# Performance work log

Measured on AMD Instinct MI355X. Metric: run time of the kernel, lower is better.

The kernel has to match this reference:

```python
import jax, jax.numpy as jnp
import numpy as np

H_FULL, W_FULL = 256, 704
IMG_H, IMG_W = 16, 44  # height//16, width//16
D_BINS, D_STR, D_END = 50, 1.0, 45.0
N_CAMS = 6
BEV_C = 192
VOX_STR = np.array([-40.0, -40.0, -1.0], np.float32)
VOX_END = np.array([40.0, 40.0, 5.4], np.float32)


def _frustum():
    # Faithful to create_pixel_grid: x/y built width-major, flattened, then flat-reshaped
    # to (img_h, img_w) in forward (this scrambling is intentional / matches torch .reshape).
    x = jnp.broadcast_to(jnp.linspace(0.0, W_FULL - 1.0, IMG_W)[:, None], (IMG_W, IMG_H))
    y = jnp.broadcast_to(jnp.linspace(0.0, H_FULL - 1.0, IMG_H)[None, :], (IMG_W, IMG_H))
    pix = jnp.stack([x, y], 0).reshape(2, IMG_H, IMG_W)
    pix = jnp.broadcast_to(pix[:, None], (2, D_BINS, IMG_H, IMG_W))
    d = jnp.broadcast_to(jnp.linspace(D_STR, D_END, D_BINS)[None, :, None, None], (1, D_BINS, IMG_H, IMG_W))
    return jnp.transpose(jnp.concatenate([pix, d], 0), (1, 2, 3, 0))  # [D, h, w, 3]


def trilinear_sample(vol, grid):
    # vol [B,C,D,H,W]; grid [B,Do,Ho,Wo,3] normalized (x,y,z); align_corners=True, zeros padding
    B, C, D, H, W = vol.shape
    Do, Ho, Wo = grid.shape[1:4]
    g = grid.reshape(B, -1, 3)
    P = g.shape[1]
    x = (g[..., 0] + 1.0) * 0.5 * (W - 1)
    y = (g[..., 1] + 1.0) * 0.5 * (H - 1)
    z = (g[..., 2] + 1.0) * 0.5 * (D - 1)
    x0f, y0f, z0f = jnp.floor(x), jnp.floor(y), jnp.floor(z)
    fx, fy, fz = x - x0f, y - y0f, z - z0f
    x0, y0, z0 = x0f.astype(jnp.int32), y0f.astype(jnp.int32), z0f.astype(jnp.int32)
    vol_flat = vol.reshape(B, C, D * H * W)
    gather = jax.vmap(lambda vf, i: jnp.take(vf, i, axis=1))
    out = jnp.zeros((B, C, P), vol.dtype)
    for dz in (0, 1):
        wz = fz if dz else 1.0 - fz
        iz = z0 + dz
        for dy in (0, 1):
            wy = fy if dy else 1.0 - fy
            iy = y0 + dy
            for dx in (0, 1):
                wx = fx if dx else 1.0 - fx
                ix = x0 + dx
                valid = (ix >= 0) & (ix < W) & (iy >= 0) & (iy < H) & (iz >= 0) & (iz < D)
                idx = (jnp.clip(iz, 0, D - 1) * H + jnp.clip(iy, 0, H - 1)) * W + jnp.clip(ix, 0, W - 1)
                v = gather(vol_flat, idx)  # [B,C,P]
                out = out + v * (wx * wy * wz * valid)[:, None, :]
    return out.reshape(B, C, Do, Ho, Wo)


def conv3x3(x, w, b):
    y = jax.lax.conv_general_dilated(x, w, window_strides=(1, 1), padding='SAME',
                                     dimension_numbers=('NCHW', 'OIHW', 'NCHW'))
    return y + b[None, :, None, None]


def setup_inputs() -> dict:
    key = jax.random.key(0)
    ks = jax.random.split(key, 10)
    B = 2
    eye3 = jnp.eye(3, dtype=jnp.float32)
    eye4 = jnp.eye(4, dtype=jnp.float32)
    bev_feat = jax.random.normal(ks[0], (B, BEV_C, 100, 100, 8), jnp.float32)
    imgs = jax.random.normal(ks[1], (B, N_CAMS, 3, H_FULL, W_FULL), jnp.float32)
    sensor2egos = eye4 + 0.1 * jax.random.normal(ks[2], (B, N_CAMS, 4, 4), jnp.float32)
    ego2globals = eye4 + 0.1 * jax.random.normal(ks[3], (B, N_CAMS, 4, 4), jnp.float32)
    K = jnp.array([[700.0, 0.0, 352.0], [0.0, 700.0, 128.0], [0.0, 0.0, 1.0]], jnp.float32)
    intrins = K + 1.0 * jax.random.normal(ks[4], (B, N_CAMS, 3, 3), jnp.float32)
    post_rots = eye3 + 0.01 * jax.random.normal(ks[5], (B, N_CAMS, 3, 3), jnp.float32)
    post_trans = 0.1 * jax.random.normal(ks[6], (B, N_CAMS, 3), jnp.float32)
    bda = eye3 + 0.01 * jax.random.normal(ks[7], (B, 3, 3), jnp.float32)
    enc = BEV_C * D_BINS  # 9600
    conv1_w = 0.003 * jax.random.normal(ks[8], (256, enc, 3, 3), jnp.float32)
    conv1_b = jnp.zeros((256,), jnp.float32)
    conv2_w = 0.02 * jax.random.normal(ks[9], (88, 256, 3, 3), jnp.float32)
    conv2_b = jnp.zeros((88,), jnp.float32)
    return dict(bev_feat=bev_feat, imgs=imgs, sensor2egos=sensor2egos, ego2globals=ego2globals,
                intrins=intrins, post_rots=post_rots, post_trans=post_trans, bda=bda,
                conv1_w=conv1_w, conv1_b=conv1_b, conv2_w=conv2_w, conv2_b=conv2_b)


def reference(bev_feat, imgs, sensor2egos, ego2globals, intrins, post_rots, post_trans, bda,
              conv1_w, conv1_b, conv2_w, conv2_b):
    B = imgs.shape[0]
    vol = jnp.transpose(bev_feat, (0, 1, 4, 3, 2))  # [B,C,Z,Y,X] -> grid_sample (x=W, y=H, z=D)
    fr = _frustum()[None, None]  # [1,1,D,h,w,3]
    pts = fr - post_trans[:, :, None, None, None, :]  # [B,6,D,h,w,3]
    pts = jnp.einsum('bnij,bndhwj->bndhwi', jnp.linalg.inv(post_rots), pts)
    pts = jnp.concatenate([pts[..., :2] * pts[..., 2:3], pts[..., 2:3]], -1)
    pts = jnp.einsum('bnij,bndhwj->bndhwi', jnp.linalg.inv(intrins[:, :N_CAMS]), pts)
    N = D_BINS * IMG_H * IMG_W
    cam = pts.reshape(B, N_CAMS, 3, N)  # faithful flat reshape (same semantics as torch .reshape)
    cam = jnp.concatenate([cam, jnp.ones((B, N_CAMS, 1, N), cam.dtype)], 2)
    ego = jnp.einsum('bnij,bnjp->bnip', sensor2egos[:, :N_CAMS, :3, :], cam)
    ego = jnp.einsum('bij,bnjp->bnip', bda, ego)
    g = jnp.transpose(ego, (0, 1, 3, 2))  # [B,6,N,3]
    vs = jnp.asarray(VOX_STR)
    vl = jnp.asarray(VOX_END - VOX_STR)
    g = (g - vs) / vl * 2.0 - 1.0
    g = g.reshape(B, N_CAMS * D_BINS, IMG_H, IMG_W, 3)  # batch all cams into the depth axis
    s = trilinear_sample(vol, g)  # [B,C,6*D,h,w]
    s = s.reshape(B, BEV_C, N_CAMS, D_BINS, IMG_H, IMG_W)
    s = jnp.transpose(s, (0, 2, 1, 3, 4, 5)).reshape(B * N_CAMS, BEV_C * D_BINS, IMG_H, IMG_W)
    x = jax.nn.relu(conv3x3(s, conv1_w, conv1_b))
    x = jax.nn.relu(conv3x3(x, conv2_w, conv2_b))
    return x  # [B*6, 88, 16, 44] == stack(dim=1).flatten(0,1)
```

## Files before the change

kernel.cpp:

```cpp
#include <hip/hip_runtime.h>
#include <hip/hip_bf16.h>
#include <stdint.h>

typedef __attribute__((ext_vector_type(8))) short s16x8;
typedef __attribute__((ext_vector_type(4))) float f32x4;
#define BF16 __hip_bfloat16

__device__ __forceinline__ void gload16(void* lds, const void* g) {
  __builtin_amdgcn_global_load_lds((const __attribute__((address_space(1))) void*)g,
                                   (__attribute__((address_space(3))) void*)lds, 16, 0, 0);
}

__device__ __forceinline__ void inv3(const float* m, float* o) {
  float a00=m[0],a01=m[1],a02=m[2],a10=m[3],a11=m[4],a12=m[5],a20=m[6],a21=m[7],a22=m[8];
  float c00 = a11*a22 - a12*a21;
  float c01 = a12*a20 - a10*a22;
  float c02 = a10*a21 - a11*a20;
  float det = a00*c00 + a01*c01 + a02*c02;
  float id = 1.0f/det;
  o[0]=c00*id; o[1]=(a02*a21-a01*a22)*id; o[2]=(a01*a12-a02*a11)*id;
  o[3]=c01*id; o[4]=(a00*a22-a02*a20)*id; o[5]=(a02*a10-a00*a12)*id;
  o[6]=c02*id; o[7]=(a01*a20-a00*a21)*id; o[8]=(a00*a11-a01*a10)*id;
}

__global__ __launch_bounds__(192) void k_prep_vol(const float* __restrict__ bev, BF16* __restrict__ volT) {
  int blk = blockIdx.x;
  int b = blk / 10000, xy = blk % 10000;
  int t = threadIdx.x;
  __shared__ alignas(16) BF16 sm[1536];
  const float* src = bev + (((size_t)b*192 + t)*10000 + xy)*8;
#pragma unroll
  for (int z = 0; z < 8; ++z) sm[z*192 + t] = __float2bfloat16(src[z]);
  __syncthreads();
  BF16* dst = volT + (size_t)blk*1536;
  *reinterpret_cast<s16x8*>(&dst[t*8]) = *reinterpret_cast<const s16x8*>(&sm[t*8]);
}

__global__ __launch_bounds__(256) void k_prep_w1(const float* __restrict__ w1, BF16* __restrict__ A1) {
  unsigned o = blockIdx.x*256u + threadIdx.x;
  unsigned oc = o / 86400u; unsigned r = o % 86400u;
  unsigned seg = r / 9600u; unsigned r2 = r % 9600u;
  unsigned dd = r2 / 192u;  unsigned c  = r2 % 192u;
  unsigned in = (oc*9600u + c*50u + dd)*9u + seg;
  A1[o] = __float2bfloat16(w1[in]);
}

__global__ __launch_bounds__(256) void k_prep_w2(const float* __restrict__ w2, BF16* __restrict__ w2T) {
  unsigned o = blockIdx.x*256u + threadIdx.x;
  unsigned oc = o / 2304u; unsigned r = o % 2304u;
  unsigned seg = r / 256u; unsigned c = r % 256u;
  float v = (oc < 88u) ? w2[(oc*256u + c)*9u + seg] : 0.0f;
  w2T[o] = __float2bfloat16(v);
}

__global__ __launch_bounds__(256) void k_geom(const float* __restrict__ s2e, const float* __restrict__ intr,
                       const float* __restrict__ prots, const float* __restrict__ ptrans,
                       const float* __restrict__ bda, float* __restrict__ geom) {
  int tid = blockIdx.x*256 + threadIdx.x;
  int p = tid % 35200; int bn = tid / 35200;
  int b = bn / 6;
  float PR[9], IN[9], iPR[9], iIN[9], BD[9], SE[12], PT[3];
#pragma unroll
  for (int i = 0; i < 9; ++i) { PR[i] = prots[bn*9+i]; IN[i] = intr[bn*9+i]; BD[i] = bda[b*9+i]; }
#pragma unroll
  for (int i = 0; i < 12; ++i) SE[i] = s2e[bn*16+i];
#pragma unroll
  for (int i = 0; i < 3; ++i) PT[i] = ptrans[bn*3+i];
  inv3(PR, iPR); inv3(IN, iIN);
  float cam[3];
#pragma unroll
  for (int c3 = 0; c3 < 3; ++c3) {
    int f = c3*35200 + p;
    int comp = f % 3; int t1 = f / 3;
    int w = t1 % 44;  int t2 = t1 / 44;
    int h = t2 % 16;  int dd = t2 / 16;
    int hw = h*44 + w;
    float px = 703.0f*(float)(hw >> 4)*(1.0f/43.0f);
    float py = 17.0f*(float)(hw & 15);
    float dv = 1.0f + 44.0f*(float)dd*(1.0f/49.0f);
    float t0 = px - PT[0], t1f = py - PT[1], t2f = dv - PT[2];
    float ux = iPR[0]*t0 + iPR[1]*t1f + iPR[2]*t2f;
    float uy = iPR[3]*t0 + iPR[4]*t1f + iPR[5]*t2f;
    float uz = iPR[6]*t0 + iPR[7]*t1f + iPR[8]*t2f;
    float m0 = ux*uz, m1 = uy*uz, m2 = uz;
    cam[c3] = iIN[comp*3+0]*m0 + iIN[comp*3+1]*m1 + iIN[comp*3+2]*m2;
  }
  float e0 = SE[0]*cam[0] + SE[1]*cam[1] + SE[2]*cam[2] + SE[3];
  float e1 = SE[4]*cam[0] + SE[5]*cam[1] + SE[6]*cam[2] + SE[7];
  float e2 = SE[8]*cam[0] + SE[9]*cam[1] + SE[10]*cam[2] + SE[11];
  float q0 = BD[0]*e0 + BD[1]*e1 + BD[2]*e2;
  float q1 = BD[3]*e0 + BD[4]*e1 + BD[5]*e2;
  float q2 = BD[6]*e0 + BD[7]*e1 + BD[8]*e2;
  float gx = (q0 + 40.0f)*(1.0f/80.0f)*2.0f - 1.0f;
  float gy = (q1 + 40.0f)*(1.0f/80.0f)*2.0f - 1.0f;
  float gz = (q2 + 1.0f)*(1.0f/6.4f)*2.0f - 1.0f;
  float* o = geom + (size_t)tid*3;
  o[0] = (gx + 1.0f)*0.5f*99.0f;
  o[1] = (gy + 1.0f)*0.5f*99.0f;
  o[2] = (gz + 1.0f)*0.5f*7.0f;
}

__global__ __launch_bounds__(256) void k_sample(const BF16* __restrict__ volT, const float* __restrict__ geom,
                         BF16* __restrict__ s_p) {
  unsigned tid = blockIdx.x*256u + threadIdx.x;
  unsigned c = tid % 192u; unsigned q = tid / 192u;
  unsigned pix = q % 704u; unsigned q2 = q / 704u;
  unsigned dd = q2 % 50u;  unsigned bn = q2 / 50u;
  unsigned b = bn / 6u;
  const float* g = geom + ((size_t)bn*35200 + dd*704 + pix)*3;
  float X = g[0], Y = g[1], Z = g[2];
  float xf = floorf(X), yf = floorf(Y), zf = floorf(Z);
  int x0 = (int)xf, y0 = (int)yf, z0 = (int)zf;
  float fx = X - xf, fy = Y - yf, fz = Z - zf;
  float acc = 0.0f;
#pragma unroll
  for (int dz = 0; dz < 2; ++dz) {
    int iz = z0 + dz; float wz = dz ? fz : 1.0f - fz;
    bool vz = (iz >= 0) && (iz < 8);
    int cz = min(max(iz, 0), 7);
#pragma unroll
    for (int dy = 0; dy < 2; ++dy) {
      int iy = y0 + dy; float wy = dy ? fy : 1.0f - fy;
      bool vy = vz && (iy >= 0) && (iy < 100);
      int cy = min(max(iy, 0), 99);
#pragma unroll
      for (int dx = 0; dx < 2; ++dx) {
        int ix = x0 + dx; float wx = dx ? fx : 1.0f - fx;
        bool vv = vy && (ix >= 0) && (ix < 100);
        int cx = min(max(ix, 0), 99);
        float wgt = wx*wy*wz;
        if (vv && wgt != 0.0f) {
          size_t a = ((((size_t)b*100 + cx)*100 + cy)*8 + cz)*192 + c;
          acc += wgt * __bfloat162float(volT[a]);
        }
      }
    }
  }
  s_p[((size_t)bn*704 + pix)*9600 + dd*192 + c] = __float2bfloat16(acc);
}

__global__ __launch_bounds__(256) void k_gemm1(const BF16* __restrict__ A1, const BF16* __restrict__ s_p,
                        const BF16* __restrict__ zpage, float* __restrict__ part) {
  int gid = blockIdx.x;
  int ks = gid % 12; int t0 = gid / 12;
  int nt = t0 % 6;   t0 /= 6;
  int mt = t0 & 1;   int bn = t0 >> 1;
  int oc0 = mt*128, pix0 = nt*128;
  int tid = threadIdx.x, wv = tid >> 6, lane = tid & 63;
  int wr = wv >> 1, wc = wv & 1;
  __shared__ alignas(16) short lA[4096];
  __shared__ alignas(16) short lB[4096];
  int rsub = lane >> 2, kcol = (lane & 3)*8;
  int lr = lane & 15, kh8 = (lane >> 4)*8;
  int k = ks*7200, kend = k + 7200;
  int arow0 = (wv*2+0)*16 + rsub;
  int arow1 = (wv*2+1)*16 + rsub;
  const BF16* gA0 = A1 + (size_t)(oc0 + arow0)*86400 + k + kcol;
  const BF16* gA1 = A1 + (size_t)(oc0 + arow1)*86400 + k + kcol;
  short* ldsA0 = &lA[(wv*2+0)*512];
  short* ldsA1 = &lA[(wv*2+1)*512];
  short* ldsB0 = &lB[(wv*2+0)*512];
  short* ldsB1 = &lB[(wv*2+1)*512];
  int prow0 = pix0 + (wv*2+0)*16 + rsub;
  int prow1 = pix0 + (wv*2+1)*16 + rsub;
  int ph00 = prow0/44, pw00 = prow0%44;
  int ph10 = prow1/44, pw10 = prow1%44;
  f32x4 acc[4][4] = {};
  while (k < kend) {
    int seg = k / 9600;
    int kloc = k - seg*9600;
    int rem0 = 9600 - kloc, rem1 = kend - k;
    int nsteps = ((rem0 < rem1) ? rem0 : rem1) >> 5;
    int dh = seg/3 - 1, dw = seg%3 - 1;
    const BF16 *gB0, *gB1; int inc0, inc1;
    {
      int ph = ph00 + dh, pw = pw00 + dw;
      bool v = (prow0 < 704) && (ph >= 0) && (ph < 16) && (pw >= 0) && (pw < 44);
      gB0 = v ? s_p + ((size_t)bn*704 + ph*44 + pw)*9600 + kloc + kcol : zpage + kcol;
      inc0 = v ? 32 : 0;
    }
    {
      int ph = ph10 + dh, pw = pw10 + dw;
      bool v = (prow1 < 704) && (ph >= 0) && (ph < 16) && (pw >= 0) && (pw < 44);
      gB1 = v ? s_p + ((size_t)bn*704 + ph*44 + pw)*9600 + kloc + kcol : zpage + kcol;
      inc1 = v ? 32 : 0;
    }
    for (int s = 0; s < nsteps; ++s) {
      __syncthreads();
      gload16(ldsA0, gA0); gload16(ldsA1, gA1);
      gload16(ldsB0, gB0); gload16(ldsB1, gB1);
      __syncthreads();
      s16x8 af[4], bfr[4];
#pragma unroll
      for (int m = 0; m < 4; ++m)
        af[m] = *reinterpret_cast<const s16x8*>(&lA[(wr*64 + m*16 + lr)*32 + kh8]);
#pragma unroll
      for (int n = 0; n < 4; ++n)
        bfr[n] = *reinterpret_cast<const s16x8*>(&lB[(wc*64 + n*16 + lr)*32 + kh8]);
#pragma unroll
      for (int m = 0; m < 4; ++m)
#pragma unroll
        for (int n = 0; n < 4; ++n)
          acc[m][n] = __builtin_amdgcn_mfma_f32_16x16x32_bf16(af[m], bfr[n], acc[m][n], 0, 0, 0);
      gA0 += 32; gA1 += 32; gB0 += inc0; gB1 += inc1;
    }
    k += nsteps*32;
  }
#pragma unroll
  for (int m = 0; m < 4; ++m) {
    int ocb = oc0 + wr*64 + m*16 + ((lane >> 4) << 2);
#pragma unroll
    for (int n = 0; n < 4; ++n) {
      int px = pix0 + wc*64 + n*16 + lr;
      if (px < 704) {
        float* dst = part + (((size_t)ks*12 + bn)*256 + ocb)*704 + px;
#pragma unroll
        for (int r = 0; r < 4; ++r) dst[(size_t)r*704] = acc[m][n][r];
      }
    }
  }
}

__global__ __launch_bounds__(256) void k_reduce1(const float* __restrict__ part, const float* __restrict__ b1,
                          BF16* __restrict__ out1p) {
  int bn = blockIdx.x / 44; int pg = blockIdx.x % 44; int pix0 = pg*16;
  int t = threadIdx.x;
  __shared__ float sm[4096];
  for (int f = t; f < 4096; f += 256) {
    int oc = f >> 4, pl = f & 15;
    float s = 0.0f;
#pragma unroll
    for (int ks = 0; ks < 12; ++ks)
      s += part[(((size_t)ks*12 + bn)*256 + oc)*704 + pix0 + pl];
    s += b1[oc];
    sm[f] = fmaxf(s, 0.0f);
  }
  __syncthreads();
  for (int f = t; f < 4096; f += 256) {
    int pl = f >> 8;
    int oc = f & 255;
    out1p[((size_t)bn*704 + pix0 + pl)*256 + oc] = __float2bfloat16(sm[oc*16 + pl]);
  }
}

__global__ __launch_bounds__(256) void k_gemm2(const BF16* __restrict__ w2T, const BF16* __restrict__ x1,
                        const BF16* __restrict__ zpage, const float* __restrict__ b2,
                        float* __restrict__ out) {
  int gid = blockIdx.x;
  int nt = gid % 11, bn = gid / 11;
  int pix0 = nt*64;
  int tid = threadIdx.x, wv = tid >> 6, lane = tid & 63;
  int wr = wv >> 1, wc = wv & 1;
  __shared__ alignas(16) short lA[3072];
  __shared__ alignas(16) short lB[2048];
  int rsub = lane >> 2, kcol = (lane & 3)*8;
  int lr = lane & 15, kh8 = (lane >> 4)*8;
  int ar0 = wv*16 + rsub;
  int ar1 = (wv+4)*16 + rsub;
  const BF16* gA0 = w2T + (size_t)ar0*2304 + kcol;
  const BF16* gA1 = w2T + (size_t)ar1*2304 + kcol;
  short* lA0 = &lA[wv*512];
  short* lA1 = &lA[(wv+4)*512];
  short* lB0 = &lB[wv*512];
  int prow = pix0 + wv*16 + rsub;
  int ph0 = prow/44, pw0 = prow%44;
  f32x4 acc[3][2] = {};
  for (int seg = 0; seg < 9; ++seg) {
    int dh = seg/3 - 1, dw = seg%3 - 1;
    int ph = ph0 + dh, pw = pw0 + dw;
    bool v = (ph >= 0) && (ph < 16) && (pw >= 0) && (pw < 44);
    const BF16* gB = v ? x1 + ((size_t)bn*704 + ph*44 + pw)*256 + kcol : zpage + kcol;
    int incB = v ? 32 : 0;
#pragma unroll
    for (int s = 0; s < 8; ++s) {
      __syncthreads();
      gload16(lA0, gA0);
      if (wv < 2) gload16(lA1, gA1);
      gload16(lB0, gB);
      __syncthreads();
      s16x8 af[3], bfr[2];
#pragma unroll
      for (int m = 0; m < 3; ++m)
        af[m] = *reinterpret_cast<const s16x8*>(&lA[(wr*48 + m*16 + lr)*32 + kh8]);
#pragma unroll
      for (int n = 0; n < 2; ++n)
        bfr[n] = *reinterpret_cast<const s16x8*>(&lB[(wc*32 + n*16 + lr)*32 + kh8]);
#pragma unroll
      for (int m = 0; m < 3; ++m)
#pragma unroll
        for (int n = 0; n < 2; ++n)
          acc[m][n] = __builtin_amdgcn_mfma_f32_16x16x32_bf16(af[m], bfr[n], acc[m][n], 0, 0, 0);
      gA0 += 32; gA1 += 32; gB += incB;
    }
  }
#pragma unroll
  for (int m = 0; m < 3; ++m) {
    int ocb = wr*48 + m*16 + ((lane >> 4) << 2);
#pragma unroll
    for (int n = 0; n < 2; ++n) {
      int px = pix0 + wc*32 + n*16 + lr;
#pragma unroll
      for (int r = 0; r < 4; ++r) {
        int oc = ocb + r;
        if (oc < 88)
          out[((size_t)bn*88 + oc)*704 + px] = fmaxf(acc[m][n][r] + b2[oc], 0.0f);
      }
    }
  }
}

extern "C" void kernel_launch(void* const* d_in, const int* in_sizes, int n_in,
                              void* d_out, int out_size, void* d_ws, size_t ws_size,
                              hipStream_t stream) {
  (void)in_sizes; (void)n_in; (void)out_size;
  const float* bev   = (const float*)d_in[0];
  const float* s2e   = (const float*)d_in[2];
  const float* intr  = (const float*)d_in[4];
  const float* prots = (const float*)d_in[5];
  const float* ptrns = (const float*)d_in[6];
  const float* bda   = (const float*)d_in[7];
  const float* w1    = (const float*)d_in[8];
  const float* b1    = (const float*)d_in[9];
  const float* w2    = (const float*)d_in[10];
  const float* b2    = (const float*)d_in[11];
  float* out = (float*)d_out;

  char* ws = (char*)d_ws;
  size_t off = 0;
  BF16*  volT  = (BF16*)(ws + off);  off += 61440000;
  BF16*  A1    = (BF16*)(ws + off);  off += 44236800;
  BF16*  w2T   = (BF16*)(ws + off);  off += 442368;
  float* geom  = (float*)(ws + off); off += 5068800;
  BF16*  s_p   = (BF16*)(ws + off);  off += 162201600;
  float* part  = (float*)(ws + off); off += 103809024;
  BF16*  out1p = (BF16*)(ws + off);  off += 4325376;
  BF16*  zpage = (BF16*)(ws + off);  off += 4096;
  if (off > ws_size) return;

  hipMemsetAsync(zpage, 0, 4096, stream);

  k_prep_vol<<<20000, 192, 0, stream>>>(bev, volT);
  k_prep_w1 <<<86400, 256, 0, stream>>>(w1, A1);
  k_prep_w2 <<<864,   256, 0, stream>>>(w2, w2T);
  k_geom    <<<1650,  256, 0, stream>>>(s2e, intr, prots, ptrns, bda, geom);
  k_sample  <<<316800,256, 0, stream>>>(volT, geom, s_p);
  k_gemm1   <<<1728,  256, 0, stream>>>(A1, s_p, zpage, part);
  k_reduce1 <<<528,   256, 0, stream>>>(part, b1, out1p);
  k_gemm2   <<<132,   256, 0, stream>>>(w2T, out1p, zpage, b2, out);
}
```

Measured before the change: 1.206 ms.

## Double-buffer gemm1, vectorize sampling and weight prep, store fp16 partials

```diff
diff --git a/kernel.cpp b/kernel.cpp
--- a/kernel.cpp
+++ b/kernel.cpp
@@ -1,14 +1,21 @@
 #include <hip/hip_runtime.h>
 #include <hip/hip_bf16.h>
+#include <hip/hip_fp16.h>
 #include <stdint.h>
 
 typedef __attribute__((ext_vector_type(8))) short s16x8;
 typedef __attribute__((ext_vector_type(4))) float f32x4;
 #define BF16 __hip_bfloat16
 
+#define VM0 asm volatile("s_waitcnt vmcnt(0)" ::: "memory")
+
 __device__ __forceinline__ void gload16(void* lds, const void* g) {
   __builtin_amdgcn_global_load_lds((const __attribute__((address_space(1))) void*)g,
                                    (__attribute__((address_space(3))) void*)lds, 16, 0, 0);
+}
+
+__device__ __forceinline__ short f2bf(float f) {
+  union { __hip_bfloat16 h; short s; } u; u.h = __float2bfloat16(f); return u.s;
 }
 
 __device__ __forceinline__ void inv3(const float* m, float* o) {
@@ -37,12 +44,36 @@
 }
 
 __global__ __launch_bounds__(256) void k_prep_w1(const float* __restrict__ w1, BF16* __restrict__ A1) {
-  unsigned o = blockIdx.x*256u + threadIdx.x;
-  unsigned oc = o / 86400u; unsigned r = o % 86400u;
-  unsigned seg = r / 9600u; unsigned r2 = r % 9600u;
-  unsigned dd = r2 / 192u;  unsigned c  = r2 % 192u;
-  unsigned in = (oc*9600u + c*50u + dd)*9u + seg;
-  A1[o] = __float2bfloat16(w1[in]);
+  int blk = blockIdx.x;
+  int oc = blk / 6, c0 = (blk % 6) * 32;
+  __shared__ short sm[18000];
+  int t = threadIdx.x;
+  const float* src = w1 + (size_t)oc*86400 + (size_t)c0*450;
+  for (int i = 0; i < 15; ++i) {
+    int f4 = i*256 + t;
+    if (f4 < 3600) {
+      float4 v = *((const float4*)src + f4);
+      int flat = f4*4;
+#pragma unroll
+      for (int q = 0; q < 4; ++q) {
+        int fl = flat + q;
+        int c = fl / 450, r = fl % 450, dd = r / 9, sg = r % 9;
+        float vq = (q==0)?v.x:(q==1)?v.y:(q==2)?v.z:v.w;
+        sm[(sg*50 + dd)*40 + c] = f2bf(vq);
+      }
+    }
+  }
+  __syncthreads();
+  BF16* dstbase = A1 + (size_t)oc*86400 + c0;
+  for (int i = 0; i < 8; ++i) {
+    int fw = i*256 + t;
+    if (fw < 1800) {
+      int sdd = fw >> 2, q4 = fw & 3;
+      int sg = sdd / 50, dd = sdd % 50;
+      s16x8 v = *(const s16x8*)&sm[sdd*40 + q4*8];
+      *(s16x8*)&dstbase[(size_t)sg*9600 + dd*192 + q4*8] = v;
+    }
+  }
 }
 
 __global__ __launch_bounds__(256) void k_prep_w2(const float* __restrict__ w2, BF16* __restrict__ w2T) {
@@ -103,16 +134,17 @@
 __global__ __launch_bounds__(256) void k_sample(const BF16* __restrict__ volT, const float* __restrict__ geom,
                          BF16* __restrict__ s_p) {
   unsigned tid = blockIdx.x*256u + threadIdx.x;
-  unsigned c = tid % 192u; unsigned q = tid / 192u;
-  unsigned pix = q % 704u; unsigned q2 = q / 704u;
-  unsigned dd = q2 % 50u;  unsigned bn = q2 / 50u;
+  unsigned cg8 = (tid % 24u) * 8u;
+  unsigned q   = tid / 24u;
+  unsigned dd  = q % 50u;  unsigned q2 = q / 50u;
+  unsigned pix = q2 % 704u; unsigned bn = q2 / 704u;
   unsigned b = bn / 6u;
   const float* g = geom + ((size_t)bn*35200 + dd*704 + pix)*3;
   float X = g[0], Y = g[1], Z = g[2];
   float xf = floorf(X), yf = floorf(Y), zf = floorf(Z);
   int x0 = (int)xf, y0 = (int)yf, z0 = (int)zf;
   float fx = X - xf, fy = Y - yf, fz = Z - zf;
-  float acc = 0.0f;
+  float acc[8] = {0,0,0,0,0,0,0,0};
 #pragma unroll
   for (int dz = 0; dz < 2; ++dz) {
     int iz = z0 + dz; float wz = dz ? fz : 1.0f - fz;
@@ -130,98 +162,101 @@
         int cx = min(max(ix, 0), 99);
         float wgt = wx*wy*wz;
         if (vv && wgt != 0.0f) {
-          size_t a = ((((size_t)b*100 + cx)*100 + cy)*8 + cz)*192 + c;
-          acc += wgt * __bfloat162float(volT[a]);
+          s16x8 v = *(const s16x8*)&volT[((((size_t)b*100 + cx)*100 + cy)*8 + cz)*192 + cg8];
+#pragma unroll
+          for (int j = 0; j < 8; ++j) {
+            unsigned u = (unsigned)(unsigned short)v[j];
+            acc[j] += wgt * __uint_as_float(u << 16);
+          }
         }
       }
     }
   }
-  s_p[((size_t)bn*704 + pix)*9600 + dd*192 + c] = __float2bfloat16(acc);
-}
-
+  s16x8 o;
+#pragma unroll
+  for (int j = 0; j < 8; ++j) o[j] = f2bf(acc[j]);
+  *(s16x8*)&s_p[((size_t)bn*704 + pix)*9600 + dd*192 + cg8] = o;
+}
+
+#define G1_NS 180
 __global__ __launch_bounds__(256) void k_gemm1(const BF16* __restrict__ A1, const BF16* __restrict__ s_p,
-                        const BF16* __restrict__ zpage, float* __restrict__ part) {
+                        const BF16* __restrict__ zpage, __half* __restrict__ part) {
   int gid = blockIdx.x;
-  int ks = gid % 12; int t0 = gid / 12;
+  int ks = gid % 15; int t0 = gid / 15;
   int nt = t0 % 6;   t0 /= 6;
   int mt = t0 & 1;   int bn = t0 >> 1;
   int oc0 = mt*128, pix0 = nt*128;
   int tid = threadIdx.x, wv = tid >> 6, lane = tid & 63;
   int wr = wv >> 1, wc = wv & 1;
-  __shared__ alignas(16) short lA[4096];
-  __shared__ alignas(16) short lB[4096];
-  int rsub = lane >> 2, kcol = (lane & 3)*8;
-  int lr = lane & 15, kh8 = (lane >> 4)*8;
-  int k = ks*7200, kend = k + 7200;
-  int arow0 = (wv*2+0)*16 + rsub;
-  int arow1 = (wv*2+1)*16 + rsub;
-  const BF16* gA0 = A1 + (size_t)(oc0 + arow0)*86400 + k + kcol;
-  const BF16* gA1 = A1 + (size_t)(oc0 + arow1)*86400 + k + kcol;
-  short* ldsA0 = &lA[(wv*2+0)*512];
-  short* ldsA1 = &lA[(wv*2+1)*512];
-  short* ldsB0 = &lB[(wv*2+0)*512];
-  short* ldsB1 = &lB[(wv*2+1)*512];
-  int prow0 = pix0 + (wv*2+0)*16 + rsub;
-  int prow1 = pix0 + (wv*2+1)*16 + rsub;
-  int ph00 = prow0/44, pw00 = prow0%44;
-  int ph10 = prow1/44, pw10 = prow1%44;
+  __shared__ alignas(16) short lA0s[4096], lA1s[4096], lB0s[4096], lB1s[4096];
+  int lr15 = lane & 15, kq8 = (lane >> 4)*8;
+  int k0 = ks*5760;
+  const BF16* gA0 = A1 + (size_t)(oc0 + wv*32 + lr15)*86400 + k0 + kq8;
+  const BF16* gA1 = gA0 + (size_t)16*86400;
+  int prow0 = pix0 + wv*32 + lr15;
+  int prow1 = prow0 + 16;
+  int ph0p = prow0/44, pw0p = prow0%44;
+  int ph1p = prow1/44, pw1p = prow1%44;
+  int seg  = k0 / 9600;
+  int kloc = k0 - seg*9600;
+  const BF16 *gB0, *gB1; int inc0, inc1;
+  {
+    int dh = seg/3 - 1, dw = seg%3 - 1;
+    { int qh = ph0p+dh, qw = pw0p+dw;
+      bool v = (prow0<704)&&(qh>=0)&&(qh<16)&&(qw>=0)&&(qw<44);
+      gB0 = v ? s_p + ((size_t)bn*704 + qh*44+qw)*9600 + kloc + kq8 : zpage + kq8; inc0 = v?32:0; }
+    { int qh = ph1p+dh, qw = pw1p+dw;
+      bool v = (prow1<704)&&(qh>=0)&&(qh<16)&&(qw>=0)&&(qw<44);
+      gB1 = v ? s_p + ((size_t)bn*704 + qh*44+qw)*9600 + kloc + kq8 : zpage + kq8; inc1 = v?32:0; }
+  }
+#define G1_STAGE(LA, LB) { gload16(&LA[wv*1024], gA0); gload16(&LA[wv*1024+512], gA1); \
+                           gload16(&LB[wv*1024], gB0); gload16(&LB[wv*1024+512], gB1); }
+#define G1_BUMP() { gA0 += 32; gA1 += 32; gB0 += inc0; gB1 += inc1; kloc += 32; \
+    if (kloc == 9600) { kloc = 0; seg++; int sg = seg < 9 ? seg : 8; \
+      int dh = sg/3 - 1, dw = sg%3 - 1; \
+      { int qh = ph0p+dh, qw = pw0p+dw; bool v = (prow0<704)&&(qh>=0)&&(qh<16)&&(qw>=0)&&(qw<44); \
+        gB0 = v ? s_p + ((size_t)bn*704 + qh*44+qw)*9600 + kq8 : zpage + kq8; inc0 = v?32:0; } \
+      { int qh = ph1p+dh, qw = pw1p+dw; bool v = (prow1<704)&&(qh>=0)&&(qh<16)&&(qw>=0)&&(qw<44); \
+        gB1 = v ? s_p + ((size_t)bn*704 + qh*44+qw)*9600 + kq8 : zpage + kq8; inc1 = v?32:0; } } }
   f32x4 acc[4][4] = {};
-  while (k < kend) {
-    int seg = k / 9600;
-    int kloc = k - seg*9600;
-    int rem0 = 9600 - kloc, rem1 = kend - k;
-    int nsteps = ((rem0 < rem1) ? rem0 : rem1) >> 5;
-    int dh = seg/3 - 1, dw = seg%3 - 1;
-    const BF16 *gB0, *gB1; int inc0, inc1;
-    {
-      int ph = ph00 + dh, pw = pw00 + dw;
-      bool v = (prow0 < 704) && (ph >= 0) && (ph < 16) && (pw >= 0) && (pw < 44);
-      gB0 = v ? s_p + ((size_t)bn*704 + ph*44 + pw)*9600 + kloc + kcol : zpage + kcol;
-      inc0 = v ? 32 : 0;
-    }
-    {
-      int ph = ph10 + dh, pw = pw10 + dw;
-      bool v = (prow1 < 704) && (ph >= 0) && (ph < 16) && (pw >= 0) && (pw < 44);
-      gB1 = v ? s_p + ((size_t)bn*704 + ph*44 + pw)*9600 + kloc + kcol : zpage + kcol;
-      inc1 = v ? 32 : 0;
-    }
-    for (int s = 0; s < nsteps; ++s) {
-      __syncthreads();
-      gload16(ldsA0, gA0); gload16(ldsA1, gA1);
-      gload16(ldsB0, gB0); gload16(ldsB1, gB1);
-      __syncthreads();
-      s16x8 af[4], bfr[4];
-#pragma unroll
-      for (int m = 0; m < 4; ++m)
-        af[m] = *reinterpret_cast<const s16x8*>(&lA[(wr*64 + m*16 + lr)*32 + kh8]);
-#pragma unroll
-      for (int n = 0; n < 4; ++n)
-        bfr[n] = *reinterpret_cast<const s16x8*>(&lB[(wc*64 + n*16 + lr)*32 + kh8]);
-#pragma unroll
-      for (int m = 0; m < 4; ++m)
-#pragma unroll
-        for (int n = 0; n < 4; ++n)
-          acc[m][n] = __builtin_amdgcn_mfma_f32_16x16x32_bf16(af[m], bfr[n], acc[m][n], 0, 0, 0);
-      gA0 += 32; gA1 += 32; gB0 += inc0; gB1 += inc1;
-    }
-    k += nsteps*32;
+  int ra = wr*2048 + lane*8;
+  int rb = wc*2048 + lane*8;
+#define G1_COMPUTE(LA, LB) { s16x8 af[4], bfv[4]; \
+    _Pragma("unroll") for (int m = 0; m < 4; ++m) af[m]  = *(const s16x8*)&LA[ra + m*512]; \
+    _Pragma("unroll") for (int n = 0; n < 4; ++n) bfv[n] = *(const s16x8*)&LB[rb + n*512]; \
+    _Pragma("unroll") for (int m = 0; m < 4; ++m) \
+    _Pragma("unroll") for (int n = 0; n < 4; ++n) \
+      acc[m][n] = __builtin_amdgcn_mfma_f32_16x16x32_bf16(af[m], bfv[n], acc[m][n], 0, 0, 0); }
+
+  G1_STAGE(lA0s, lB0s); G1_BUMP();
+  VM0;
+  __syncthreads();
+  for (int t = 0; t < G1_NS; t += 2) {
+    G1_STAGE(lA1s, lB1s); G1_BUMP();
+    G1_COMPUTE(lA0s, lB0s);
+    VM0;
+    __syncthreads();
+    if (t + 2 < G1_NS) { G1_STAGE(lA0s, lB0s); G1_BUMP(); }
+    G1_COMPUTE(lA1s, lB1s);
+    VM0;
+    __syncthreads();
   }
 #pragma unroll
   for (int m = 0; m < 4; ++m) {
     int ocb = oc0 + wr*64 + m*16 + ((lane >> 4) << 2);
 #pragma unroll
     for (int n = 0; n < 4; ++n) {
-      int px = pix0 + wc*64 + n*16 + lr;
+      int px = pix0 + wc*64 + n*16 + lr15;
       if (px < 704) {
-        float* dst = part + (((size_t)ks*12 + bn)*256 + ocb)*704 + px;
-#pragma unroll
-        for (int r = 0; r < 4; ++r) dst[(size_t)r*704] = acc[m][n][r];
+        __half* dst = part + (((size_t)ks*12 + bn)*256 + ocb)*704 + px;
+#pragma unroll
+        for (int r = 0; r < 4; ++r) dst[(size_t)r*704] = __float2half(acc[m][n][r]);
       }
     }
   }
 }
 
-__global__ __launch_bounds__(256) void k_reduce1(const float* __restrict__ part, const float* __restrict__ b1,
+__global__ __launch_bounds__(256) void k_reduce1(const __half* __restrict__ part, const float* __restrict__ b1,
                           BF16* __restrict__ out1p) {
   int bn = blockIdx.x / 44; int pg = blockIdx.x % 44; int pix0 = pg*16;
   int t = threadIdx.x;
@@ -230,8 +265,8 @@
     int oc = f >> 4, pl = f & 15;
     float s = 0.0f;
 #pragma unroll
-    for (int ks = 0; ks < 12; ++ks)
-      s += part[(((size_t)ks*12 + bn)*256 + oc)*704 + pix0 + pl];
+    for (int ks = 0; ks < 15; ++ks)
+      s += __half2float(part[(((size_t)ks*12 + bn)*256 + oc)*704 + pix0 + pl]);
     s += b1[oc];
     sm[f] = fmaxf(s, 0.0f);
   }
@@ -253,43 +288,35 @@
   int wr = wv >> 1, wc = wv & 1;
   __shared__ alignas(16) short lA[3072];
   __shared__ alignas(16) short lB[2048];
-  int rsub = lane >> 2, kcol = (lane & 3)*8;
-  int lr = lane & 15, kh8 = (lane >> 4)*8;
-  int ar0 = wv*16 + rsub;
-  int ar1 = (wv+4)*16 + rsub;
-  const BF16* gA0 = w2T + (size_t)ar0*2304 + kcol;
-  const BF16* gA1 = w2T + (size_t)ar1*2304 + kcol;
-  short* lA0 = &lA[wv*512];
-  short* lA1 = &lA[(wv+4)*512];
-  short* lB0 = &lB[wv*512];
-  int prow = pix0 + wv*16 + rsub;
+  int lr15 = lane & 15, kq8 = (lane >> 4)*8;
+  const BF16* gA0 = w2T + (size_t)(wv*16 + lr15)*2304 + kq8;
+  const BF16* gA1 = w2T + (size_t)((4+wv)*16 + lr15)*2304 + kq8;
+  int prow = pix0 + wv*16 + lr15;
   int ph0 = prow/44, pw0 = prow%44;
   f32x4 acc[3][2] = {};
   for (int seg = 0; seg < 9; ++seg) {
     int dh = seg/3 - 1, dw = seg%3 - 1;
-    int ph = ph0 + dh, pw = pw0 + dw;
-    bool v = (ph >= 0) && (ph < 16) && (pw >= 0) && (pw < 44);
-    const BF16* gB = v ? x1 + ((size_t)bn*704 + ph*44 + pw)*256 + kcol : zpage + kcol;
+    int qh = ph0 + dh, qw = pw0 + dw;
+    bool v = (qh >= 0) && (qh < 16) && (qw >= 0) && (qw < 44);
+    const BF16* gB = v ? x1 + ((size_t)bn*704 + qh*44 + qw)*256 + kq8 : zpage + kq8;
     int incB = v ? 32 : 0;
-#pragma unroll
     for (int s = 0; s < 8; ++s) {
       __syncthreads();
-      gload16(lA0, gA0);
-      if (wv < 2) gload16(lA1, gA1);
-      gload16(lB0, gB);
+      gload16(&lA[wv*512], gA0);
+      if (wv < 2) gload16(&lA[(4+wv)*512], gA1);
+      gload16(&lB[wv*512], gB);
+      VM0;
       __syncthreads();
-      s16x8 af[3], bfr[2];
+      s16x8 af[3], bfv[2];
+#pragma unroll
+      for (int m = 0; m < 3; ++m) af[m]  = *(const s16x8*)&lA[(wr*3+m)*512 + lane*8];
+#pragma unroll
+      for (int n = 0; n < 2; ++n) bfv[n] = *(const s16x8*)&lB[(wc*2+n)*512 + lane*8];
 #pragma unroll
       for (int m = 0; m < 3; ++m)
-        af[m] = *reinterpret_cast<const s16x8*>(&lA[(wr*48 + m*16 + lr)*32 + kh8]);
-#pragma unroll
-      for (int n = 0; n < 2; ++n)
-        bfr[n] = *reinterpret_cast<const s16x8*>(&lB[(wc*32 + n*16 + lr)*32 + kh8]);
-#pragma unroll
-      for (int m = 0; m < 3; ++m)
 #pragma unroll
         for (int n = 0; n < 2; ++n)
-          acc[m][n] = __builtin_amdgcn_mfma_f32_16x16x32_bf16(af[m], bfr[n], acc[m][n], 0, 0, 0);
+          acc[m][n] = __builtin_amdgcn_mfma_f32_16x16x32_bf16(af[m], bfv[n], acc[m][n], 0, 0, 0);
       gA0 += 32; gA1 += 32; gB += incB;
     }
   }
@@ -298,7 +325,7 @@
     int ocb = wr*48 + m*16 + ((lane >> 4) << 2);
 #pragma unroll
     for (int n = 0; n < 2; ++n) {
-      int px = pix0 + wc*32 + n*16 + lr;
+      int px = pix0 + wc*32 + n*16 + lr15;
 #pragma unroll
       for (int r = 0; r < 4; ++r) {
         int oc = ocb + r;
@@ -327,24 +354,24 @@
 
   char* ws = (char*)d_ws;
   size_t off = 0;
-  BF16*  volT  = (BF16*)(ws + off);  off += 61440000;
-  BF16*  A1    = (BF16*)(ws + off);  off += 44236800;
-  BF16*  w2T   = (BF16*)(ws + off);  off += 442368;
-  float* geom  = (float*)(ws + off); off += 5068800;
-  BF16*  s_p   = (BF16*)(ws + off);  off += 162201600;
-  float* part  = (float*)(ws + off); off += 103809024;
-  BF16*  out1p = (BF16*)(ws + off);  off += 4325376;
-  BF16*  zpage = (BF16*)(ws + off);  off += 4096;
+  BF16*   volT  = (BF16*)(ws + off);   off += 61440000;
+  BF16*   A1    = (BF16*)(ws + off);   off += 44236800;
+  BF16*   w2T   = (BF16*)(ws + off);   off += 442368;
+  float*  geom  = (float*)(ws + off);  off += 5068800;
+  BF16*   s_p   = (BF16*)(ws + off);   off += 162201600;
+  __half* part  = (__half*)(ws + off); off += 64880640;
+  BF16*   out1p = (BF16*)(ws + off);   off += 4325376;
+  BF16*   zpage = (BF16*)(ws + off);   off += 4096;
   if (off > ws_size) return;
 
   hipMemsetAsync(zpage, 0, 4096, stream);
 
   k_prep_vol<<<20000, 192, 0, stream>>>(bev, volT);
-  k_prep_w1 <<<86400, 256, 0, stream>>>(w1, A1);
+  k_prep_w1 <<<1536,  256, 0, stream>>>(w1, A1);
   k_prep_w2 <<<864,   256, 0, stream>>>(w2, w2T);
   k_geom    <<<1650,  256, 0, stream>>>(s2e, intr, prots, ptrns, bda, geom);
-  k_sample  <<<316800,256, 0, stream>>>(volT, geom, s_p);
-  k_gemm1   <<<1728,  256, 0, stream>>>(A1, s_p, zpage, part);
+  k_sample  <<<39600, 256, 0, stream>>>(volT, geom, s_p);
+  k_gemm1   <<<2160,  256, 0, stream>>>(A1, s_p, zpage, part);
   k_reduce1 <<<528,   256, 0, stream>>>(part, b1, out1p);
   k_gemm2   <<<132,   256, 0, stream>>>(w2T, out1p, zpage, b2, out);
 }
```

Result: slower. 1.334 ms (+10.6%).
